# Kernel optimization log

Measured on AMD Instinct MI355X. Metric: run time of the kernel, lower is better.

Reference implementation:

```python
import jax, jax.numpy as jnp
import numpy as np

N_NODES = 50000
N_EDGES = 600000
D_FEAT = 128
HIDDEN = 128
N_CLASSES = 40
K_HOPS = 2


def setup_inputs() -> dict:
    key = jax.random.key(0)
    k_x, k_e, k_w1, k_b1, k_w2, k_b2 = jax.random.split(key, 6)
    x = jax.random.normal(k_x, (N_NODES, D_FEAT), dtype=jnp.float32)
    edge_index = jax.random.randint(k_e, (2, N_EDGES), 0, N_NODES, dtype=jnp.int64)
    # SGConv linear (applied after K-hop propagation) and classifier, Glorot-ish init
    W_sgc = jax.random.normal(k_w1, (D_FEAT, HIDDEN), dtype=jnp.float32) / np.sqrt(D_FEAT)
    b_sgc = jnp.zeros((HIDDEN,), dtype=jnp.float32)
    W_cls = jax.random.normal(k_w2, (HIDDEN, N_CLASSES), dtype=jnp.float32) / np.sqrt(HIDDEN)
    b_cls = jnp.zeros((N_CLASSES,), dtype=jnp.float32)
    return {"x": x, "edge_index": edge_index, "W_sgc": W_sgc, "b_sgc": b_sgc,
            "W_cls": W_cls, "b_cls": b_cls}


def _gcn_norm(edge_index, num_nodes):
    # Add self-loops (PyG SGConv default), compute symmetric GCN normalization.
    loops = jnp.arange(num_nodes, dtype=edge_index.dtype)
    src = jnp.concatenate([edge_index[0], loops])  # [E+N]
    dst = jnp.concatenate([edge_index[1], loops])  # [E+N]
    deg = jax.ops.segment_sum(jnp.ones_like(dst, dtype=jnp.float32), dst,
                              num_segments=num_nodes)
    dinv = jnp.where(deg > 0, jax.lax.rsqrt(deg), 0.0)
    norm = dinv[src] * dinv[dst]  # [E+N]
    return src, dst, norm


def reference(x, edge_index, W_sgc, b_sgc, W_cls, b_cls):
    num_nodes = x.shape[0]
    src, dst, norm = _gcn_norm(edge_index, num_nodes)
    h = x
    for _ in range(K_HOPS):  # K-hop propagation: h <- D^-1/2 (A+I) D^-1/2 h
        h = jax.ops.segment_sum(norm[:, None] * h[src], dst, num_segments=num_nodes)
    h = h @ W_sgc + b_sgc          # SGConv's trailing linear
    # F.dropout with training=False is identity (inference); skip.
    out = h @ W_cls + b_cls        # classifier
    return out
```

## Files before the change

### kernel.cpp

```cpp
#include <hip/hip_runtime.h>
#include <hip/hip_fp16.h>

#define N_NODES 50000
#define N_EDGES 600000
#define D 128
#define NC 40
#define BUCKET_CAP 96
#define NPART 8
#define PART_SZ (N_NODES / NPART)
#define E4 (N_EDGES / 4)
#define FUSE_ELEMS (D * NC + NC)

#define ZERO_BLKS ((N_NODES / 4 + 255) / 256)
#define FUSE_BLKS ((FUSE_ELEMS + 255) / 256)
#define CMP_BLKS ((E4 + 255) / 256)
#define K0B (ZERO_BLKS + FUSE_BLKS + CMP_BLKS)

#define FILLB 1024
#define PROJB ((N_NODES + 63) / 64)
#define K1B (FILLB + PROJB)

#define PULLB ((N_NODES + 47) / 48)

typedef int v4i __attribute__((ext_vector_type(4)));
typedef _Float16 hf2 __attribute__((ext_vector_type(2)));
typedef float vf2 __attribute__((ext_vector_type(2)));

struct alignas(16) H8 { __half2 h[4]; };
struct alignas(8)  H4 { __half2 h[2]; };
struct alignas(16) HV4 { hf2 h[4]; };

__device__ __forceinline__ float4 h4f(H4 v) {
    float2 p = __half22float2(v.h[0]), q = __half22float2(v.h[1]);
    return make_float4(p.x, p.y, q.x, q.y);
}


__global__ void k_prep(int4* __restrict__ cnt4,
                       const float* __restrict__ Wsgc, const float* __restrict__ bsgc,
                       const float* __restrict__ Wcls, const float* __restrict__ bcls,
                       float* __restrict__ Wf, float* __restrict__ bf,
                       const v4i* __restrict__ src4, const v4i* __restrict__ dst4,
                       v4i* __restrict__ packed4) {
    int b = blockIdx.x, t = threadIdx.x;
    if (b < ZERO_BLKS) {
        int i = b * 256 + t;
        if (i < N_NODES / 4) cnt4[i] = make_int4(0, 0, 0, 0);
    } else if (b < ZERO_BLKS + FUSE_BLKS) {
        int idx = (b - ZERO_BLKS) * 256 + t;
        if (idx < D * NC) {
            int k = idx / NC, c = idx % NC;
            float acc = 0.f;
            for (int j = 0; j < D; j++) acc += Wsgc[k * D + j] * Wcls[j * NC + c];
            Wf[idx] = acc;
        } else if (idx < FUSE_ELEMS) {
            int c = idx - D * NC;
            float acc = bcls[c];
            for (int j = 0; j < D; j++) acc += bsgc[j] * Wcls[j * NC + c];
            bf[c] = acc;
        }
    } else {
        int i = (b - ZERO_BLKS - FUSE_BLKS) * 256 + t;
        if (i < E4) {
            v4i d = __builtin_nontemporal_load(&dst4[i]);
            v4i s = __builtin_nontemporal_load(&src4[i]);
            v4i p;
            p.x = (int)(((unsigned)d.x << 16) | (unsigned)s.x);
            p.y = (int)(((unsigned)d.y << 16) | (unsigned)s.y);
            p.z = (int)(((unsigned)d.z << 16) | (unsigned)s.z);
            p.w = (int)(((unsigned)d.w << 16) | (unsigned)s.w);
            packed4[i] = p;
        }
    }
}


__global__ __launch_bounds__(320) void k_fill_proj(
    const v4i* __restrict__ packed4, int* __restrict__ cnt,
    unsigned short* __restrict__ bucket,
    const float* __restrict__ x, const float* __restrict__ Wf,
    __half* __restrict__ z) {
    __shared__ hf2 sW[64][40];
    __shared__ hf2 sX[64][65];
    int t = threadIdx.x, b = blockIdx.x;
    if (b < FILLB) {
        int part = b & (NPART - 1);
        int bip  = b >> 3;
        int lo = part * PART_SZ, hi = lo + PART_SZ;
        const int stride = (FILLB >> 3) * 320;
        for (int i = bip * 320 + t; i < E4; i += stride) {
            v4i p = packed4[i];
#define FO(pp)                                                             \
            {                                                              \
                int d = (int)(((unsigned)(pp)) >> 16);                     \
                if (d >= lo && d < hi) {                                   \
                    int pos = atomicAdd(&cnt[d], 1);                       \
                    if (pos < BUCKET_CAP)                                  \
                        bucket[(size_t)d * BUCKET_CAP + pos] =             \
                            (unsigned short)((pp) & 0xFFFF);               \
                }                                                          \
            }
            FO(p.x) FO(p.y) FO(p.z) FO(p.w)
#undef FO
        }
        return;
    }
    for (int i = t; i < 64 * 40; i += 320) {
        int k2 = i / 40, c = i - k2 * 40;
        hf2 w;
        w.x = (_Float16)Wf[(2 * k2) * NC + c];
        w.y = (_Float16)Wf[(2 * k2 + 1) * NC + c];
        sW[k2][c] = w;
    }
    int base = (b - FILLB) * 64;
    int rows = N_NODES - base;
    if (rows > 64) rows = 64;
    const vf2* xs = reinterpret_cast<const vf2*>(x + (size_t)base * D);
    for (int i = t; i < rows * 64; i += 320) {
        vf2 v = __builtin_nontemporal_load(&xs[i]);
        hf2 h;
        h.x = (_Float16)v.x;
        h.y = (_Float16)v.y;
        sX[i >> 6][i & 63] = h;
    }
    __syncthreads();
    int lane = t & 63;
    int wv = t >> 6;
    int c0 = wv * 8;
    int node = base + lane;
    if (node >= N_NODES) return;
    float a0 = 0.f, a1 = 0.f, a2 = 0.f, a3 = 0.f;
    float a4 = 0.f, a5 = 0.f, a6 = 0.f, a7 = 0.f;
#pragma unroll 8
    for (int k2 = 0; k2 < 64; k2++) {
        hf2 hx = sX[lane][k2];
        HV4 wa = *reinterpret_cast<const HV4*>(&sW[k2][c0]);
        HV4 wb = *reinterpret_cast<const HV4*>(&sW[k2][c0 + 4]);
#if __has_builtin(__builtin_amdgcn_fdot2)
        a0 = __builtin_amdgcn_fdot2(hx, wa.h[0], a0, false);
        a1 = __builtin_amdgcn_fdot2(hx, wa.h[1], a1, false);
        a2 = __builtin_amdgcn_fdot2(hx, wa.h[2], a2, false);
        a3 = __builtin_amdgcn_fdot2(hx, wa.h[3], a3, false);
        a4 = __builtin_amdgcn_fdot2(hx, wb.h[0], a4, false);
        a5 = __builtin_amdgcn_fdot2(hx, wb.h[1], a5, false);
        a6 = __builtin_amdgcn_fdot2(hx, wb.h[2], a6, false);
        a7 = __builtin_amdgcn_fdot2(hx, wb.h[3], a7, false);
#else
        float xl = (float)hx.x, xh = (float)hx.y;
        a0 += xl * (float)wa.h[0].x + xh * (float)wa.h[0].y;
        a1 += xl * (float)wa.h[1].x + xh * (float)wa.h[1].y;
        a2 += xl * (float)wa.h[2].x + xh * (float)wa.h[2].y;
        a3 += xl * (float)wa.h[3].x + xh * (float)wa.h[3].y;
        a4 += xl * (float)wb.h[0].x + xh * (float)wb.h[0].y;
        a5 += xl * (float)wb.h[1].x + xh * (float)wb.h[1].y;
        a6 += xl * (float)wb.h[2].x + xh * (float)wb.h[2].y;
        a7 += xl * (float)wb.h[3].x + xh * (float)wb.h[3].y;
#endif
    }
    H8 o;
    o.h[0] = __floats2half2_rn(a0, a1);
    o.h[1] = __floats2half2_rn(a2, a3);
    o.h[2] = __floats2half2_rn(a4, a5);
    o.h[3] = __floats2half2_rn(a6, a7);
    *reinterpret_cast<H8*>(z + (size_t)node * NC + c0) = o;
}


template <int MODE>
__global__ __launch_bounds__(512) void k_pull(const int* __restrict__ cnt,
                                              const unsigned short* __restrict__ bucket,
                                              const __half* __restrict__ hin,
                                              void* __restrict__ houtv,
                                              const float* __restrict__ bias) {
    int wave = threadIdx.x >> 6;
    int lane = threadIdx.x & 63;
    int g = lane / 10;
    int l = lane - g * 10;
    int node = blockIdx.x * 48 + wave * 6 + g;
    if (g >= 6 || node >= N_NODES) return;
    int f = l << 2;
    int c = cnt[node];
    int n = c < BUCKET_CAP ? c : BUCKET_CAP;
    float di = rsqrtf((float)c + 1.0f);
    float4 acc = h4f(*reinterpret_cast<const H4*>(hin + (size_t)node * NC + f));
    if (MODE == 0) { acc.x *= di; acc.y *= di; acc.z *= di; acc.w *= di; }
    const unsigned short* bk = bucket + (size_t)node * BUCKET_CAP;
    int j = 0;
    for (; j + 4 <= n; j += 4) {
        int s0 = bk[j], s1 = bk[j + 1], s2 = bk[j + 2], s3 = bk[j + 3];
        float4 v0 = h4f(*reinterpret_cast<const H4*>(hin + (size_t)s0 * NC + f));
        float4 v1 = h4f(*reinterpret_cast<const H4*>(hin + (size_t)s1 * NC + f));
        float4 v2 = h4f(*reinterpret_cast<const H4*>(hin + (size_t)s2 * NC + f));
        float4 v3 = h4f(*reinterpret_cast<const H4*>(hin + (size_t)s3 * NC + f));
        if (MODE == 0) {
            float w0 = rsqrtf((float)cnt[s0] + 1.0f);
            float w1 = rsqrtf((float)cnt[s1] + 1.0f);
            float w2 = rsqrtf((float)cnt[s2] + 1.0f);
            float w3 = rsqrtf((float)cnt[s3] + 1.0f);
            acc.x += w0 * v0.x + w1 * v1.x + w2 * v2.x + w3 * v3.x;
            acc.y += w0 * v0.y + w1 * v1.y + w2 * v2.y + w3 * v3.y;
            acc.z += w0 * v0.z + w1 * v1.z + w2 * v2.z + w3 * v3.z;
            acc.w += w0 * v0.w + w1 * v1.w + w2 * v2.w + w3 * v3.w;
        } else {
            acc.x += v0.x + v1.x + v2.x + v3.x;
            acc.y += v0.y + v1.y + v2.y + v3.y;
            acc.z += v0.z + v1.z + v2.z + v3.z;
            acc.w += v0.w + v1.w + v2.w + v3.w;
        }
    }
    for (; j < n; j++) {
        int s0 = bk[j];
        float4 v0 = h4f(*reinterpret_cast<const H4*>(hin + (size_t)s0 * NC + f));
        float w0 = (MODE == 0) ? rsqrtf((float)cnt[s0] + 1.0f) : 1.0f;
        acc.x += w0 * v0.x; acc.y += w0 * v0.y; acc.z += w0 * v0.z; acc.w += w0 * v0.w;
    }
    if (MODE == 0) {
        float sc = di * di;
        __half* ho = (__half*)houtv;
        H4 o;
        o.h[0] = __floats2half2_rn(sc * acc.x, sc * acc.y);
        o.h[1] = __floats2half2_rn(sc * acc.z, sc * acc.w);
        *reinterpret_cast<H4*>(ho + (size_t)node * NC + f) = o;
    } else {
        float* ho = (float*)houtv;
        float4 b = *reinterpret_cast<const float4*>(bias + f);
        acc.x = di * acc.x + b.x; acc.y = di * acc.y + b.y;
        acc.z = di * acc.z + b.z; acc.w = di * acc.w + b.w;
        *reinterpret_cast<float4*>(ho + (size_t)node * NC + f) = acc;
    }
}


extern "C" void kernel_launch(void* const* d_in, const int* in_sizes, int n_in,
                              void* d_out, int out_size, void* d_ws, size_t ws_size,
                              hipStream_t stream) {
    const float* x    = (const float*)d_in[0];
    const int*   ei   = (const int*)d_in[1];
    const float* Wsgc = (const float*)d_in[2];
    const float* bsgc = (const float*)d_in[3];
    const float* Wcls = (const float*)d_in[4];
    const float* bcls = (const float*)d_in[5];
    float* out = (float*)d_out;

    const v4i* src4 = (const v4i*)ei;
    const v4i* dst4 = (const v4i*)(ei + N_EDGES);

    char* ws = (char*)d_ws;
    size_t off = 0;
    auto alloc = [&](size_t bytes) -> void* {
        void* p = ws + off;
        off += (bytes + 255) & ~255ull;
        return p;
    };
    int*            cnt    = (int*)alloc((size_t)N_NODES * 4);
    unsigned short* bucket = (unsigned short*)alloc((size_t)N_NODES * BUCKET_CAP * 2);
    v4i*            packed = (v4i*)alloc((size_t)N_EDGES * 4);
    __half*         z      = (__half*)alloc((size_t)N_NODES * NC * 2);
    __half*         u1     = (__half*)alloc((size_t)N_NODES * NC * 2);
    float*          Wf     = (float*)alloc((size_t)D * NC * 4);
    float*          bf     = (float*)alloc((size_t)NC * 4);

    k_prep<<<K0B, 256, 0, stream>>>((int4*)cnt, Wsgc, bsgc, Wcls, bcls, Wf, bf,
                                    src4, dst4, (v4i*)packed);
    k_fill_proj<<<K1B, 320, 0, stream>>>((const v4i*)packed, cnt, bucket, x, Wf, z);
    k_pull<0><<<PULLB, 512, 0, stream>>>(cnt, bucket, z, (void*)u1, nullptr);
    k_pull<1><<<PULLB, 512, 0, stream>>>(cnt, bucket, u1, (void*)out, bf);
}
```

Measured before the change: 89.70 us.

## Co-schedule edge bucketing warps inside projection blocks instead of separate blocks

Replaces the separate fill blocks and projection blocks with one block type of 512 threads. Within each block, 320 threads load x and W and run the projection, while 192 threads do the partitioned edge bucketing, split into two halves around the barrier. The aim is to overlap the atomic-heavy fill work with the projection loads and compute inside the same CUs. The cost is a larger block with higher register and occupancy pressure, plus fill threads that sit idle at the barrier. The nontemporal load on x is also dropped.

```diff
diff --git a/kernel.cpp b/kernel.cpp
--- a/kernel.cpp
+++ b/kernel.cpp
@@ -9,6 +9,7 @@
 #define NPART 8
 #define PART_SZ (N_NODES / NPART)
 #define E4 (N_EDGES / 4)
+#define E4H (E4 / 2)
 #define FUSE_ELEMS (D * NC + NC)
 
 #define ZERO_BLKS ((N_NODES / 4 + 255) / 256)
@@ -16,15 +17,13 @@
 #define CMP_BLKS ((E4 + 255) / 256)
 #define K0B (ZERO_BLKS + FUSE_BLKS + CMP_BLKS)
 
-#define FILLB 1024
-#define PROJB ((N_NODES + 63) / 64)
-#define K1B (FILLB + PROJB)
+#define K1B ((N_NODES + 63) / 64)
+#define FTHR 192
 
 #define PULLB ((N_NODES + 47) / 48)
 
 typedef int v4i __attribute__((ext_vector_type(4)));
 typedef _Float16 hf2 __attribute__((ext_vector_type(2)));
-typedef float vf2 __attribute__((ext_vector_type(2)));
 
 struct alignas(16) H8 { __half2 h[4]; };
 struct alignas(8)  H4 { __half2 h[2]; };
@@ -75,7 +74,30 @@
 }
 
 
-__global__ __launch_bounds__(320) void k_fill_proj(
+__device__ __forceinline__ void fill_range(const v4i* __restrict__ packed4,
+                                           int* __restrict__ cnt,
+                                           unsigned short* __restrict__ bucket,
+                                           int gtid, int gstride,
+                                           int i0, int i1, int lo, int hi) {
+    for (int i = i0 + gtid; i < i1; i += gstride) {
+        v4i p = packed4[i];
+#define FO(pp)                                                             \
+        {                                                                  \
+            int d = (int)(((unsigned)(pp)) >> 16);                         \
+            if (d >= lo && d < hi) {                                       \
+                int pos = atomicAdd(&cnt[d], 1);                           \
+                if (pos < BUCKET_CAP)                                      \
+                    bucket[(size_t)d * BUCKET_CAP + pos] =                 \
+                        (unsigned short)((pp) & 0xFFFF);                   \
+            }                                                              \
+        }
+        FO(p.x) FO(p.y) FO(p.z) FO(p.w)
+#undef FO
+    }
+}
+
+
+__global__ __launch_bounds__(512) void k_fill_proj(
     const v4i* __restrict__ packed4, int* __restrict__ cnt,
     unsigned short* __restrict__ bucket,
     const float* __restrict__ x, const float* __restrict__ Wf,
@@ -83,47 +105,41 @@
     __shared__ hf2 sW[64][40];
     __shared__ hf2 sX[64][65];
     int t = threadIdx.x, b = blockIdx.x;
-    if (b < FILLB) {
-        int part = b & (NPART - 1);
-        int bip  = b >> 3;
-        int lo = part * PART_SZ, hi = lo + PART_SZ;
-        const int stride = (FILLB >> 3) * 320;
-        for (int i = bip * 320 + t; i < E4; i += stride) {
-            v4i p = packed4[i];
-#define FO(pp)                                                             \
-            {                                                              \
-                int d = (int)(((unsigned)(pp)) >> 16);                     \
-                if (d >= lo && d < hi) {                                   \
-                    int pos = atomicAdd(&cnt[d], 1);                       \
-                    if (pos < BUCKET_CAP)                                  \
-                        bucket[(size_t)d * BUCKET_CAP + pos] =             \
-                            (unsigned short)((pp) & 0xFFFF);               \
-                }                                                          \
-            }
-            FO(p.x) FO(p.y) FO(p.z) FO(p.w)
-#undef FO
-        }
+    int base = b * 64;
+
+    int part = b & (NPART - 1);
+    int nbip = (K1B - part + NPART - 1) / NPART;
+    int bip  = b >> 3;
+    int lo = part * PART_SZ, hi = lo + PART_SZ;
+    int gtid = bip * FTHR + (t - 320);
+    int gstride = nbip * FTHR;
+
+    if (t >= 320) {
+        fill_range(packed4, cnt, bucket, gtid, gstride, 0, E4H, lo, hi);
+    } else {
+        for (int i = t; i < 64 * 40; i += 320) {
+            int k2 = i / 40, c = i - k2 * 40;
+            hf2 w;
+            w.x = (_Float16)Wf[(2 * k2) * NC + c];
+            w.y = (_Float16)Wf[(2 * k2 + 1) * NC + c];
+            sW[k2][c] = w;
+        }
+        int rows = N_NODES - base;
+        if (rows > 64) rows = 64;
+        const float2* xs = reinterpret_cast<const float2*>(x + (size_t)base * D);
+        for (int i = t; i < rows * 64; i += 320) {
+            float2 v = xs[i];
+            hf2 h;
+            h.x = (_Float16)v.x;
+            h.y = (_Float16)v.y;
+            sX[i >> 6][i & 63] = h;
+        }
+    }
+    __syncthreads();
+    if (t >= 320) {
+        fill_range(packed4, cnt, bucket, gtid, gstride, E4H, E4, lo, hi);
         return;
     }
-    for (int i = t; i < 64 * 40; i += 320) {
-        int k2 = i / 40, c = i - k2 * 40;
-        hf2 w;
-        w.x = (_Float16)Wf[(2 * k2) * NC + c];
-        w.y = (_Float16)Wf[(2 * k2 + 1) * NC + c];
-        sW[k2][c] = w;
-    }
-    int base = (b - FILLB) * 64;
-    int rows = N_NODES - base;
-    if (rows > 64) rows = 64;
-    const vf2* xs = reinterpret_cast<const vf2*>(x + (size_t)base * D);
-    for (int i = t; i < rows * 64; i += 320) {
-        vf2 v = __builtin_nontemporal_load(&xs[i]);
-        hf2 h;
-        h.x = (_Float16)v.x;
-        h.y = (_Float16)v.y;
-        sX[i >> 6][i & 63] = h;
-    }
-    __syncthreads();
     int lane = t & 63;
     int wv = t >> 6;
     int c0 = wv * 8;
@@ -262,7 +278,7 @@
 
     k_prep<<<K0B, 256, 0, stream>>>((int4*)cnt, Wsgc, bsgc, Wcls, bcls, Wf, bf,
                                     src4, dst4, (v4i*)packed);
-    k_fill_proj<<<K1B, 320, 0, stream>>>((const v4i*)packed, cnt, bucket, x, Wf, z);
+    k_fill_proj<<<K1B, 512, 0, stream>>>((const v4i*)packed, cnt, bucket, x, Wf, z);
     k_pull<0><<<PULLB, 512, 0, stream>>>(cnt, bucket, z, (void*)u1, nullptr);
     k_pull<1><<<PULLB, 512, 0, stream>>>(cnt, bucket, u1, (void*)out, bf);
 }
```

Result: faster. 80.74 us (-10.0%).
